# Kernel tuning notes

Measured on AMD Instinct MI355X. Metric: run time of the kernel, lower is better.

## Reference

```python
import jax, jax.numpy as jnp
import numpy as np


def setup_inputs() -> dict:
    key = jax.random.key(0)
    k1, k2, k3 = jax.random.split(key, 3)
    B, C, H, Wd, p = 64, 3, 448, 448, 28
    x = jax.random.normal(k1, (B, C, H, Wd), dtype=jnp.float32)
    W = jax.random.normal(k2, (3, 3, p, p), dtype=jnp.float32) * 0.02
    b = jax.random.normal(k3, (3,), dtype=jnp.float32) * 0.02
    return {"x": x, "W": W, "b": b, "patch_size": p}


def reference(x, W, b, patch_size):
    # Conv2d(3->3, kernel=stride=patch_size) == blockwise contraction over each patch.
    B, C, H, Wd = x.shape
    p = patch_size
    Hp, Wp = H // p, Wd // p
    N = Hp * Wp
    # [B, C, Hp, p, Wp, p]
    xr = x.reshape(B, C, Hp, p, Wp, p)
    # patches: [B, 3(out), Hp, Wp]
    patches = jnp.einsum('bchiwj,ocij->bohw', xr, W) + b[None, :, None, None]
    # Bilinear upsample of a 1x1 map is a constant broadcast; mean over channels
    # commutes with the broadcast, so compute channel-mean first then broadcast.
    m = patches.mean(axis=1)  # [B, Hp, Wp]
    out = jnp.broadcast_to(m.reshape(B, N, 1, 1), (B, N, p, p))
    return out
```

## Files before the change

### kernel.cpp

```cpp
#include <hip/hip_runtime.h>


#define BLOCK 256
#define NF 588

typedef float f32x4 __attribute__((ext_vector_type(4)));

__global__ __launch_bounds__(BLOCK) void patchify_kernel(
    const float* __restrict__ x, const float* __restrict__ W,
    const float* __restrict__ bias, float* __restrict__ out) {
  __shared__ float4 sW4[NF];
  __shared__ int    sT[NF];

  const int t = threadIdx.x;

  for (int f = t; f < NF; f += BLOCK) {
    const float4 a = reinterpret_cast<const float4*>(W)[f];
    const float4 g = reinterpret_cast<const float4*>(W)[f + NF];
    const float4 h = reinterpret_cast<const float4*>(W)[f + 2 * NF];
    sW4[f] = make_float4((a.x + g.x + h.x) * (1.f / 3.f),
                         (a.y + g.y + h.y) * (1.f / 3.f),
                         (a.z + g.z + h.z) * (1.f / 3.f),
                         (a.w + g.w + h.w) * (1.f / 3.f));
    const int c   = f / 196;
    const int rem = f - c * 196;
    const int i   = rem / 7;
    const int j4  = rem - i * 7;
    sT[f] = (c * 200704 + i * 448 + j4 * 4) * 4;
  }
  __syncthreads();

  const int lane = t & 63;
  const int P    = blockIdx.x * 4 + (t >> 6);
  const int b    = P >> 8;
  const int rem  = P & 255;
  const int hp   = rem >> 4;
  const int wp   = rem & 15;

  const char* xbase = reinterpret_cast<const char*>(
      x + (size_t)b * 602112 + (size_t)(hp * 28) * 448 + wp * 28);

  float s = 0.f;
  #pragma unroll
  for (int it = 0; it < 9; ++it) {
    const int f = it * 64 + lane;
    const float4 v = *reinterpret_cast<const float4*>(xbase + sT[f]);
    const float4 w = sW4[f];
    s += v.x * w.x + v.y * w.y + v.z * w.z + v.w * w.w;
  }
  {
    const int f = 576 + lane;
    if (f < NF) {
      const float4 v = *reinterpret_cast<const float4*>(xbase + sT[f]);
      const float4 w = sW4[f];
      s += v.x * w.x + v.y * w.y + v.z * w.z + v.w * w.w;
    }
  }

  #pragma unroll
  for (int m = 32; m >= 1; m >>= 1) s += __shfl_xor(s, m, 64);
  s += (bias[0] + bias[1] + bias[2]) * (1.f / 3.f);

  f32x4* o4 = reinterpret_cast<f32x4*>(out + (size_t)P * 784);
  const f32x4 val = {s, s, s, s};
  #pragma unroll
  for (int it = 0; it < 4; ++it) {
    const int idx = it * 64 + lane;
    if (idx < 196) __builtin_nontemporal_store(val, o4 + idx);
  }
}

extern "C" void kernel_launch(void* const* d_in, const int* in_sizes, int n_in,
                              void* d_out, int out_size, void* d_ws, size_t ws_size,
                              hipStream_t stream) {
  const float* x    = (const float*)d_in[0];
  const float* W    = (const float*)d_in[1];
  const float* bias = (const float*)d_in[2];
  float* out = (float*)d_out;
  patchify_kernel<<<dim3(4096), dim3(BLOCK), 0, stream>>>(x, W, bias, out);
}
```

Measured before the change: 236.2 us.

## Stage full patch-row strips in padded LDS for coalesced input loads

Each block now handles one 28-row strip (16 patches) of one image. For each channel it copies the strip into padded shared memory with fully coalesced float4 loads, then each wave reads its patch from LDS. Before, every wave gathered scattered 112-byte segments per patch row straight from global memory. The change adds three block-wide barriers per channel and about 50KB of LDS per block, which may limit occupancy, and it serializes each load phase against its compute phase.

```diff
diff --git a/kernel.cpp b/kernel.cpp
--- a/kernel.cpp
+++ b/kernel.cpp
@@ -1,59 +1,77 @@
 #include <hip/hip_runtime.h>
 
 
-#define BLOCK 256
-#define NF 588
+#define ROWPAD 113
 
 typedef float f32x4 __attribute__((ext_vector_type(4)));
 
-__global__ __launch_bounds__(BLOCK) void patchify_kernel(
+__global__ __launch_bounds__(1024, 8) void patchify_kernel(
     const float* __restrict__ x, const float* __restrict__ W,
     const float* __restrict__ bias, float* __restrict__ out) {
-  __shared__ float4 sW4[NF];
-  __shared__ int    sT[NF];
+  __shared__ float4 sX[28 * ROWPAD];
+  __shared__ float4 sW4[588];
 
-  const int t = threadIdx.x;
+  const int t    = threadIdx.x;
+  const int lane = t & 63;
+  const int w    = t >> 6;
+  const int blk  = blockIdx.x;
+  const int b    = blk >> 4;
+  const int hp   = blk & 15;
 
-  for (int f = t; f < NF; f += BLOCK) {
-    const float4 a = reinterpret_cast<const float4*>(W)[f];
-    const float4 g = reinterpret_cast<const float4*>(W)[f + NF];
-    const float4 h = reinterpret_cast<const float4*>(W)[f + 2 * NF];
-    sW4[f] = make_float4((a.x + g.x + h.x) * (1.f / 3.f),
+  if (t < 588) {
+    const float4 a = reinterpret_cast<const float4*>(W)[t];
+    const float4 g = reinterpret_cast<const float4*>(W)[t + 588];
+    const float4 h = reinterpret_cast<const float4*>(W)[t + 1176];
+    sW4[t] = make_float4((a.x + g.x + h.x) * (1.f / 3.f),
                          (a.y + g.y + h.y) * (1.f / 3.f),
                          (a.z + g.z + h.z) * (1.f / 3.f),
                          (a.w + g.w + h.w) * (1.f / 3.f));
-    const int c   = f / 196;
-    const int rem = f - c * 196;
-    const int i   = rem / 7;
-    const int j4  = rem - i * 7;
-    sT[f] = (c * 200704 + i * 448 + j4 * 4) * 4;
   }
-  __syncthreads();
 
-  const int lane = t & 63;
-  const int P    = blockIdx.x * 4 + (t >> 6);
-  const int b    = P >> 8;
-  const int rem  = P & 255;
-  const int hp   = rem >> 4;
-  const int wp   = rem & 15;
-
-  const char* xbase = reinterpret_cast<const char*>(
-      x + (size_t)b * 602112 + (size_t)(hp * 28) * 448 + wp * 28);
+  const float4* xstrip = reinterpret_cast<const float4*>(
+      x + (size_t)b * 602112 + (size_t)(hp * 28) * 448);
 
   float s = 0.f;
-  #pragma unroll
-  for (int it = 0; it < 9; ++it) {
-    const int f = it * 64 + lane;
-    const float4 v = *reinterpret_cast<const float4*>(xbase + sT[f]);
-    const float4 w = sW4[f];
-    s += v.x * w.x + v.y * w.y + v.z * w.z + v.w * w.w;
-  }
-  {
-    const int f = 576 + lane;
-    if (f < NF) {
-      const float4 v = *reinterpret_cast<const float4*>(xbase + sT[f]);
-      const float4 w = sW4[f];
-      s += v.x * w.x + v.y * w.y + v.z * w.z + v.w * w.w;
+  for (int c = 0; c < 3; ++c) {
+    __syncthreads();
+
+    const float4* src = xstrip + (size_t)c * 50176;
+    #pragma unroll
+    for (int it = 0; it < 3; ++it) {
+      const int g    = it * 1024 + t;
+      const int i    = g / 112;
+      const int col4 = g - i * 112;
+      sX[i * ROWPAD + col4] = src[i * 112 + col4];
+    }
+    {
+      const int g = 3072 + t;
+      if (g < 3136) {
+        const int i    = g / 112;
+        const int col4 = g - i * 112;
+        sX[i * ROWPAD + col4] = src[i * 112 + col4];
+      }
+    }
+    __syncthreads();
+
+    const int wbase = c * 196;
+    #pragma unroll
+    for (int it = 0; it < 3; ++it) {
+      const int fc = it * 64 + lane;
+      const int i  = fc / 7;
+      const int j4 = fc - i * 7;
+      const float4 v  = sX[i * ROWPAD + w * 7 + j4];
+      const float4 w4 = sW4[wbase + fc];
+      s += v.x * w4.x + v.y * w4.y + v.z * w4.z + v.w * w4.w;
+    }
+    {
+      const int fc = 192 + lane;
+      if (fc < 196) {
+        const int i  = fc / 7;
+        const int j4 = fc - i * 7;
+        const float4 v  = sX[i * ROWPAD + w * 7 + j4];
+        const float4 w4 = sW4[wbase + fc];
+        s += v.x * w4.x + v.y * w4.y + v.z * w4.z + v.w * w4.w;
+      }
     }
   }
 
@@ -61,7 +79,7 @@
   for (int m = 32; m >= 1; m >>= 1) s += __shfl_xor(s, m, 64);
   s += (bias[0] + bias[1] + bias[2]) * (1.f / 3.f);
 
-  f32x4* o4 = reinterpret_cast<f32x4*>(out + (size_t)P * 784);
+  f32x4* o4 = reinterpret_cast<f32x4*>(out + ((size_t)blk * 16 + w) * 784);
   const f32x4 val = {s, s, s, s};
   #pragma unroll
   for (int it = 0; it < 4; ++it) {
@@ -77,5 +95,5 @@
   const float* W    = (const float*)d_in[1];
   const float* bias = (const float*)d_in[2];
   float* out = (float*)d_out;
-  patchify_kernel<<<dim3(4096), dim3(BLOCK), 0, stream>>>(x, W, bias, out);
+  patchify_kernel<<<dim3(1024), dim3(1024), 0, stream>>>(x, W, bias, out);
 }
```

Result: no change. 239.5 us (+1.4%).

## Split patch kernel into prep, reduce, and broadcast-write kernels

Applied to the files above, without the earlier changes.

The single fused kernel becomes three launches. The first averages the weights and bias once into workspace. The second computes each patch's dot product and writes one scalar per patch. The third broadcasts those scalars to the output with ordinary stores instead of nontemporal ones. This removes the per-block shared-memory weight preparation and the mixing of reads and writes within one kernel, at the cost of two extra launches and a round trip through workspace. Offsets are now computed with multiply-shift division instead of a shared-memory table.

```diff
diff --git a/kernel.cpp b/kernel.cpp
--- a/kernel.cpp
+++ b/kernel.cpp
@@ -1,35 +1,30 @@
 #include <hip/hip_runtime.h>
 
 
-#define BLOCK 256
-#define NF 588
-
 typedef float f32x4 __attribute__((ext_vector_type(4)));
 
-__global__ __launch_bounds__(BLOCK) void patchify_kernel(
-    const float* __restrict__ x, const float* __restrict__ W,
-    const float* __restrict__ bias, float* __restrict__ out) {
-  __shared__ float4 sW4[NF];
-  __shared__ int    sT[NF];
+#define WS_M_OFF 2560
 
+__global__ __launch_bounds__(256) void k0_prep(
+    const float* __restrict__ W, const float* __restrict__ bias,
+    float* __restrict__ ws) {
   const int t = threadIdx.x;
+  const float4* W4 = reinterpret_cast<const float4*>(W);
+  float4* o = reinterpret_cast<float4*>(ws);
+  for (int f = t; f < 588; f += 256) {
+    const float4 a = W4[f], g = W4[f + 588], h = W4[f + 1176];
+    o[f] = make_float4((a.x + g.x + h.x) * (1.f / 3.f),
+                       (a.y + g.y + h.y) * (1.f / 3.f),
+                       (a.z + g.z + h.z) * (1.f / 3.f),
+                       (a.w + g.w + h.w) * (1.f / 3.f));
+  }
+  if (t == 0) ws[2352] = (bias[0] + bias[1] + bias[2]) * (1.f / 3.f);
+}
 
-  for (int f = t; f < NF; f += BLOCK) {
-    const float4 a = reinterpret_cast<const float4*>(W)[f];
-    const float4 g = reinterpret_cast<const float4*>(W)[f + NF];
-    const float4 h = reinterpret_cast<const float4*>(W)[f + 2 * NF];
-    sW4[f] = make_float4((a.x + g.x + h.x) * (1.f / 3.f),
-                         (a.y + g.y + h.y) * (1.f / 3.f),
-                         (a.z + g.z + h.z) * (1.f / 3.f),
-                         (a.w + g.w + h.w) * (1.f / 3.f));
-    const int c   = f / 196;
-    const int rem = f - c * 196;
-    const int i   = rem / 7;
-    const int j4  = rem - i * 7;
-    sT[f] = (c * 200704 + i * 448 + j4 * 4) * 4;
-  }
-  __syncthreads();
-
+__global__ __launch_bounds__(256) void k1_reduce(
+    const float* __restrict__ x, const float* __restrict__ ws_w,
+    float* __restrict__ ws_m) {
+  const int t    = threadIdx.x;
   const int lane = t & 63;
   const int P    = blockIdx.x * 4 + (t >> 6);
   const int b    = P >> 8;
@@ -38,35 +33,52 @@
   const int wp   = rem & 15;
 
   const char* xbase = reinterpret_cast<const char*>(
-      x + (size_t)b * 602112 + (size_t)(hp * 28) * 448 + wp * 28);
+      x + (size_t)b * 602112 + (size_t)hp * 12544 + wp * 28);
+  const float4* wm4 = reinterpret_cast<const float4*>(ws_w);
 
   float s = 0.f;
   #pragma unroll
   for (int it = 0; it < 9; ++it) {
-    const int f = it * 64 + lane;
-    const float4 v = *reinterpret_cast<const float4*>(xbase + sT[f]);
-    const float4 w = sW4[f];
+    const int f  = it * 64 + lane;
+    const int c  = (f * 1339) >> 18;
+    const int r2 = f - c * 196;
+    const int i  = (r2 * 9363) >> 16;
+    const int j4 = r2 - i * 7;
+    const float4 v = *reinterpret_cast<const float4*>(
+        xbase + c * 802816 + i * 1792 + j4 * 16);
+    const float4 w = wm4[f];
     s += v.x * w.x + v.y * w.y + v.z * w.z + v.w * w.w;
   }
   {
     const int f = 576 + lane;
-    if (f < NF) {
-      const float4 v = *reinterpret_cast<const float4*>(xbase + sT[f]);
-      const float4 w = sW4[f];
+    if (f < 588) {
+      const int c  = (f * 1339) >> 18;
+      const int r2 = f - c * 196;
+      const int i  = (r2 * 9363) >> 16;
+      const int j4 = r2 - i * 7;
+      const float4 v = *reinterpret_cast<const float4*>(
+          xbase + c * 802816 + i * 1792 + j4 * 16);
+      const float4 w = wm4[f];
       s += v.x * w.x + v.y * w.y + v.z * w.z + v.w * w.w;
     }
   }
-
   #pragma unroll
   for (int m = 32; m >= 1; m >>= 1) s += __shfl_xor(s, m, 64);
-  s += (bias[0] + bias[1] + bias[2]) * (1.f / 3.f);
+  if (lane == 0) ws_m[P] = s + ws_w[2352];
+}
 
+__global__ __launch_bounds__(256) void k2_write(
+    const float* __restrict__ ws_m, float* __restrict__ out) {
+  const int t    = threadIdx.x;
+  const int lane = t & 63;
+  const int P    = blockIdx.x * 4 + (t >> 6);
+  const float s  = ws_m[P];
   f32x4* o4 = reinterpret_cast<f32x4*>(out + (size_t)P * 784);
   const f32x4 val = {s, s, s, s};
   #pragma unroll
   for (int it = 0; it < 4; ++it) {
     const int idx = it * 64 + lane;
-    if (idx < 196) __builtin_nontemporal_store(val, o4 + idx);
+    if (idx < 196) o4[idx] = val;
   }
 }
 
@@ -77,5 +89,8 @@
   const float* W    = (const float*)d_in[1];
   const float* bias = (const float*)d_in[2];
   float* out = (float*)d_out;
-  patchify_kernel<<<dim3(4096), dim3(BLOCK), 0, stream>>>(x, W, bias, out);
+  float* ws  = (float*)d_ws;
+  k0_prep <<<dim3(1),    dim3(256), 0, stream>>>(W, bias, ws);
+  k1_reduce<<<dim3(4096), dim3(256), 0, stream>>>(x, ws, ws + WS_M_OFF);
+  k2_write <<<dim3(4096), dim3(256), 0, stream>>>(ws + WS_M_OFF, out);
 }
```

After: 242.8 us. 1.03x slower.
